# Performance work log

Measured on AMD Instinct MI355X. Metric: run time of the kernel, lower is better.

Reference implementation:

```python
import math
import jax, jax.numpy as jnp
import numpy as np

H = 1024
N2 = 32  # N // 2
L_LEN = 4096


def setup_inputs() -> dict:
    key = jax.random.key(0)
    k0, k1, k2 = jax.random.split(key, 3)
    log_dt = jax.random.uniform(k0, (H,), dtype=jnp.float32) * (
        math.log(0.1) - math.log(0.001)) + math.log(0.001)
    C_real = jax.random.normal(k1, (H, N2), dtype=jnp.float32)
    C_imag = jax.random.normal(k2, (H, N2), dtype=jnp.float32)
    log_A_real = jnp.log(0.5 * jnp.ones((H, N2), dtype=jnp.float32))
    A_imag = math.pi * jnp.tile(jnp.arange(N2, dtype=jnp.float32)[None, :], (H, 1))
    return {
        "log_dt": log_dt,
        "C_real": C_real,
        "C_imag": C_imag,
        "log_A_real": log_A_real,
        "A_imag": A_imag,
        "L": L_LEN,
    }


def reference(log_dt, C_real, C_imag, log_A_real, A_imag, L):
    dt = jnp.exp(log_dt)                                   # [H]
    A = -jnp.exp(log_A_real) + 1j * A_imag                 # [H, N2] complex
    dtA = A * dt[:, None]                                  # [H, N2]
    l = jnp.arange(L, dtype=jnp.float32)                   # [L]
    Kexp = jnp.exp(dtA[:, :, None] * l)                    # [H, N2, L] complex (Vandermonde)
    Ct = (C_real + 1j * C_imag) * (jnp.exp(dtA) - 1.0) / A  # [H, N2]
    K = 2.0 * jnp.einsum('hn,hnl->hl', Ct, Kexp).real      # [H, L]
    return K
```

## Files before the change

kernel.cpp:

```cpp
#include <hip/hip_runtime.h>


#define N2    32
#define LLEN  4096
#define BLK   512
#define TQ    256
#define CL    16
#define TOL   1e-3f

typedef float v2f __attribute__((ext_vector_type(2)));

__global__ __launch_bounds__(BLK, 8) void s4d_kernel(
    const float* __restrict__ log_dt,
    const float* __restrict__ C_real,
    const float* __restrict__ C_imag,
    const float* __restrict__ log_A_real,
    const float* __restrict__ A_imag,
    float* __restrict__ out)
{
    const int h   = blockIdx.x;
    const int tid = threadIdx.x;
    const int t   = tid & (TQ - 1);
    const int sl  = tid >> 8;

    __shared__ v2f    sT0[N2][16];
    __shared__ float4 sU1[N2][16];
    __shared__ v2f    sAB[N2];
    __shared__ v2f    sCt[N2];
    __shared__ float  sDrl2[N2];
    __shared__ double sTrev[N2];
    __shared__ float  sRed[CL][TQ];
    __shared__ float  sS, sRmax, sDrmax;
    __shared__ int    sJcut;

    if (tid < N2) {
        const int n = tid;
        const float dt = __expf(log_dt[h]);
        const float aR = -__expf(log_A_real[h * N2 + n]);
        const float aI = A_imag[h * N2 + n];
        const float dR = aR * dt;

        const double trev = (double)aI * (double)dt * 0.15915494309189535;

        double pz = trev; pz -= floor(pz);
        const float e1 = __expf(dR);
        const float zr = e1 * __builtin_amdgcn_cosf((float)pz);
        const float zi = e1 * __builtin_amdgcn_sinf((float)pz);

        const float inv = 1.0f / (aR * aR + aI * aI);
        const float nr  = zr - 1.0f;
        const float qr  = (nr * aR + zi * aI) * inv;
        const float qi  = (zi * aR - nr * aI) * inv;
        const float c_r = C_real[h * N2 + n], c_i = C_imag[h * N2 + n];
        const float Ctr = c_r * qr - c_i * qi;
        const float Cti = c_r * qi + c_i * qr;

        double p256 = trev * 256.0; p256 -= floor(p256);
        const float ew = __expf(dR * 256.0f);
        const float wx = ew * __builtin_amdgcn_cosf((float)p256);
        const float r2 = ew * ew;
        const float drl2 = dR * 1.4426950408889634f;

        sCt[n]   = (v2f){Ctr, Cti};
        sDrl2[n] = drl2;
        sTrev[n] = trev;
        sAB[n]   = (v2f){2.0f * wx, -r2};

        float S = fabsf(Ctr) + fabsf(Cti);
        float r = ew;
        float dm = drl2;
#pragma unroll
        for (int m = 16; m >= 1; m >>= 1) {
            S  += __shfl_xor(S, m, 32);
            r   = fmaxf(r,  __shfl_xor(r,  m, 32));
            dm  = fmaxf(dm, __shfl_xor(dm, m, 32));
        }
        if (n == 0) {
            sS = S; sRmax = r; sDrmax = dm;
            int jc = CL;
            if (r < 0.9999f) {
                const float tail0 = 2.0f * S / (1.0f - r);
                jc = 0;
                float rj = 1.0f;
                while (jc < CL && tail0 * rj >= TOL) { rj *= r; ++jc; }
            }
            sJcut = jc;
        }
    }
    __syncthreads();

#pragma unroll
    for (int it = 0; it < 2; ++it) {
        const int tau = tid + BLK * it;
        if (tau < 512) {
            const int n = tau >> 4, k = tau & 15;
            double p = sTrev[n] * (double)k; p -= floor(p);
            const float g = __builtin_amdgcn_exp2f(sDrl2[n] * (float)k);
            sT0[n][k] = (v2f){ g * __builtin_amdgcn_cosf((float)p),
                               g * __builtin_amdgcn_sinf((float)p) };
        } else {
            const int tu = tau - 512;
            const int n = tu >> 4, m = tu & 15;
            const v2f    Ct = sCt[n];
            const double tr = sTrev[n];
            const float  dl = sDrl2[n];

            double p0 = tr * (double)(16 * m); p0 -= floor(p0);
            const float g0 = __builtin_amdgcn_exp2f(dl * (float)(16 * m));
            const float c0 = g0 * __builtin_amdgcn_cosf((float)p0);
            const float s0 = g0 * __builtin_amdgcn_sinf((float)p0);

            double p1 = tr * (double)(16 * m + 256); p1 -= floor(p1);
            const float g1 = __builtin_amdgcn_exp2f(dl * (float)(16 * m + 256));
            const float c1 = g1 * __builtin_amdgcn_cosf((float)p1);
            const float s1 = g1 * __builtin_amdgcn_sinf((float)p1);

            sU1[n][m] = make_float4(Ct.x * c0 - Ct.y * s0,
                                    Ct.x * s0 + Ct.y * c0,
                                    Ct.x * c1 - Ct.y * s1,
                                    Ct.x * s1 + Ct.y * c1);
        }
    }
    __syncthreads();

    float acc[CL];
#pragma unroll
    for (int j = 0; j < CL; ++j) acc[j] = 0.0f;

    const int jcut = __builtin_amdgcn_readfirstlane(sJcut);
    bool active = (jcut > 0);
    {
        const float rmax = sRmax;
        if (rmax < 0.9999f) {
            const float bound = 2.0f * sS *
                __builtin_amdgcn_exp2f(sDrmax * (float)t) / (1.0f - rmax);
            if (bound < TOL) active = false;
        }
    }

    if (active) {
        const int t0 = t & 15, t1 = t >> 4;
        const int nbase = sl * 16;

        for (int ch = 0; ch < 2; ++ch) {
            const int nb = nbase + ch * 8;
            float xa[8], xb[8], ca[8], cb[8];

#pragma unroll
            for (int k = 0; k < 8; ++k) {
                const int n = nb + k;
                const v2f    b = sT0[n][t0];
                const float4 u = sU1[n][t1];
                xa[k] = __builtin_fmaf(-u.y, b.y, u.x * b.x);
                xb[k] = __builtin_fmaf(-u.w, b.y, u.z * b.x);
                const v2f ab = sAB[n];
                ca[k] = ab.x;  cb[k] = ab.y;
            }

#pragma unroll
            for (int k = 0; k < 8; ++k) acc[0] += xa[k];
            if (jcut > 1) {
#pragma unroll
                for (int k = 0; k < 8; ++k) acc[1] += xb[k];
            }

#pragma unroll
            for (int jp = 0; jp < (CL - 2) / 2; ++jp) {
                const int j = 2 + 2 * jp;
                if (j < jcut) {
#pragma unroll
                    for (int k = 0; k < 8; ++k) {
                        xa[k] = ca[k] * xb[k] + cb[k] * xa[k];
                        acc[j] += xa[k];
                    }
#pragma unroll
                    for (int k = 0; k < 8; ++k) {
                        xb[k] = ca[k] * xa[k] + cb[k] * xb[k];
                        acc[j + 1] += xb[k];
                    }
                }
            }
        }
    }

    if (sl == 0) {
#pragma unroll
        for (int j = 0; j < CL; ++j) sRed[j][t] = acc[j];
    }
    __syncthreads();
    if (sl == 1) {
#pragma unroll
        for (int j = 0; j < CL; ++j) sRed[j][t] += acc[j];
    }
    __syncthreads();

    float* __restrict__ o = out + (size_t)h * LLEN + sl * (8 * TQ) + t;
#pragma unroll
    for (int jj = 0; jj < 8; ++jj)
        o[jj * TQ] = 2.0f * sRed[8 * sl + jj][t];
}

extern "C" void kernel_launch(void* const* d_in, const int* in_sizes, int n_in,
                              void* d_out, int out_size, void* d_ws, size_t ws_size,
                              hipStream_t stream) {
    const float* log_dt     = (const float*)d_in[0];
    const float* C_real     = (const float*)d_in[1];
    const float* C_imag     = (const float*)d_in[2];
    const float* log_A_real = (const float*)d_in[3];
    const float* A_imag     = (const float*)d_in[4];
    float* out = (float*)d_out;

    const int H = in_sizes[0];
    s4d_kernel<<<dim3(H), dim3(BLK), 0, stream>>>(
        log_dt, C_real, C_imag, log_A_real, A_imag, out);
}
```

Before: 88.24 us.

## Split modes across two blocks per channel and combine with atomics

Each channel's 32 modes are now split over two 256-thread blocks (2H blocks total). Each block writes its partial sums straight to global memory with atomicAdd after the output is zeroed with a memset, replacing the shared-memory reduction and its barriers. The setup stage is also trimmed: U1 is derived from U0 by multiplying with the precomputed w = z^256 rather than doing a second exp/sincos, and the per-mode tables are packed in pairs into float4 for wider LDS reads. In exchange this adds a memset launch, global atomic traffic, and outputs beyond jcut that are left at zero from the memset.

```diff
diff --git a/kernel.cpp b/kernel.cpp
--- a/kernel.cpp
+++ b/kernel.cpp
@@ -1,11 +1,11 @@
 #include <hip/hip_runtime.h>
 
 
-#define N2    32
 #define LLEN  4096
-#define BLK   512
-#define TQ    256
+#define BLK   256
 #define CL    16
+#define NB    16
+#define NPB   8
 #define TOL   1e-3f
 
 typedef float v2f __attribute__((ext_vector_type(2)));
@@ -18,26 +18,26 @@
     const float* __restrict__ A_imag,
     float* __restrict__ out)
 {
-    const int h   = blockIdx.x;
-    const int tid = threadIdx.x;
-    const int t   = tid & (TQ - 1);
-    const int sl  = tid >> 8;
-
-    __shared__ v2f    sT0[N2][16];
-    __shared__ float4 sU1[N2][16];
-    __shared__ v2f    sAB[N2];
-    __shared__ v2f    sCt[N2];
-    __shared__ float  sDrl2[N2];
-    __shared__ double sTrev[N2];
-    __shared__ float  sRed[CL][TQ];
+    const int bx    = blockIdx.x;
+    const int h     = bx & 1023;
+    const int half  = bx >> 10;
+    const int nbase = half * NB;
+    const int t     = threadIdx.x;
+
+    __shared__ float4 sT0P[NPB][16];
+    __shared__ float4 sU1[NB][16];
+    __shared__ float4 sABP[NPB];
+    __shared__ v2f    sCt[NB], sW[NB];
+    __shared__ float  sDrl2[NB];
+    __shared__ double sTrev[NB];
     __shared__ float  sS, sRmax, sDrmax;
     __shared__ int    sJcut;
 
-    if (tid < N2) {
-        const int n = tid;
+    if (t < NB) {
+        const int n  = h * 32 + nbase + t;
         const float dt = __expf(log_dt[h]);
-        const float aR = -__expf(log_A_real[h * N2 + n]);
-        const float aI = A_imag[h * N2 + n];
+        const float aR = -__expf(log_A_real[n]);
+        const float aI = A_imag[n];
         const float dR = aR * dt;
 
         const double trev = (double)aI * (double)dt * 0.15915494309189535;
@@ -51,31 +51,35 @@
         const float nr  = zr - 1.0f;
         const float qr  = (nr * aR + zi * aI) * inv;
         const float qi  = (zi * aR - nr * aI) * inv;
-        const float c_r = C_real[h * N2 + n], c_i = C_imag[h * N2 + n];
+        const float c_r = C_real[n], c_i = C_imag[n];
         const float Ctr = c_r * qr - c_i * qi;
         const float Cti = c_r * qi + c_i * qr;
 
         double p256 = trev * 256.0; p256 -= floor(p256);
         const float ew = __expf(dR * 256.0f);
         const float wx = ew * __builtin_amdgcn_cosf((float)p256);
+        const float wy = ew * __builtin_amdgcn_sinf((float)p256);
         const float r2 = ew * ew;
         const float drl2 = dR * 1.4426950408889634f;
 
-        sCt[n]   = (v2f){Ctr, Cti};
-        sDrl2[n] = drl2;
-        sTrev[n] = trev;
-        sAB[n]   = (v2f){2.0f * wx, -r2};
-
-        float S = fabsf(Ctr) + fabsf(Cti);
-        float r = ew;
+        sCt[t]   = (v2f){Ctr, Cti};
+        sW[t]    = (v2f){wx, wy};
+        sDrl2[t] = drl2;
+        sTrev[t] = trev;
+        float* ab = (float*)&sABP[t >> 1];
+        ab[t & 1]       = 2.0f * wx;
+        ab[2 + (t & 1)] = -r2;
+
+        float S  = fabsf(Ctr) + fabsf(Cti);
+        float r  = ew;
         float dm = drl2;
 #pragma unroll
-        for (int m = 16; m >= 1; m >>= 1) {
-            S  += __shfl_xor(S, m, 32);
-            r   = fmaxf(r,  __shfl_xor(r,  m, 32));
-            dm  = fmaxf(dm, __shfl_xor(dm, m, 32));
-        }
-        if (n == 0) {
+        for (int m = 8; m >= 1; m >>= 1) {
+            S  += __shfl_xor(S, m, 16);
+            r   = fmaxf(r,  __shfl_xor(r,  m, 16));
+            dm  = fmaxf(dm, __shfl_xor(dm, m, 16));
+        }
+        if (t == 0) {
             sS = S; sRmax = r; sDrmax = dm;
             int jc = CL;
             if (r < 0.9999f) {
@@ -89,37 +93,27 @@
     }
     __syncthreads();
 
-#pragma unroll
-    for (int it = 0; it < 2; ++it) {
-        const int tau = tid + BLK * it;
-        if (tau < 512) {
-            const int n = tau >> 4, k = tau & 15;
-            double p = sTrev[n] * (double)k; p -= floor(p);
-            const float g = __builtin_amdgcn_exp2f(sDrl2[n] * (float)k);
-            sT0[n][k] = (v2f){ g * __builtin_amdgcn_cosf((float)p),
-                               g * __builtin_amdgcn_sinf((float)p) };
-        } else {
-            const int tu = tau - 512;
-            const int n = tu >> 4, m = tu & 15;
-            const v2f    Ct = sCt[n];
-            const double tr = sTrev[n];
-            const float  dl = sDrl2[n];
-
-            double p0 = tr * (double)(16 * m); p0 -= floor(p0);
-            const float g0 = __builtin_amdgcn_exp2f(dl * (float)(16 * m));
-            const float c0 = g0 * __builtin_amdgcn_cosf((float)p0);
-            const float s0 = g0 * __builtin_amdgcn_sinf((float)p0);
-
-            double p1 = tr * (double)(16 * m + 256); p1 -= floor(p1);
-            const float g1 = __builtin_amdgcn_exp2f(dl * (float)(16 * m + 256));
-            const float c1 = g1 * __builtin_amdgcn_cosf((float)p1);
-            const float s1 = g1 * __builtin_amdgcn_sinf((float)p1);
-
-            sU1[n][m] = make_float4(Ct.x * c0 - Ct.y * s0,
-                                    Ct.x * s0 + Ct.y * c0,
-                                    Ct.x * c1 - Ct.y * s1,
-                                    Ct.x * s1 + Ct.y * c1);
-        }
+    {
+        const int nl = t >> 4, k = t & 15;
+        double p = sTrev[nl] * (double)k; p -= floor(p);
+        const float g  = __builtin_amdgcn_exp2f(sDrl2[nl] * (float)k);
+        const float re = g * __builtin_amdgcn_cosf((float)p);
+        const float im = g * __builtin_amdgcn_sinf((float)p);
+        float* dst = (float*)&sT0P[nl >> 1][k] + (nl & 1) * 2;
+        dst[0] = re; dst[1] = im;
+
+        const int m = k;
+        double pu = sTrev[nl] * (double)(16 * m); pu -= floor(pu);
+        const float gu = __builtin_amdgcn_exp2f(sDrl2[nl] * (float)(16 * m));
+        const float c0 = gu * __builtin_amdgcn_cosf((float)pu);
+        const float s0 = gu * __builtin_amdgcn_sinf((float)pu);
+        const v2f Ct = sCt[nl];
+        const v2f w  = sW[nl];
+        const float u0r = Ct.x * c0 - Ct.y * s0;
+        const float u0i = Ct.x * s0 + Ct.y * c0;
+        const float u1r = u0r * w.x - u0i * w.y;
+        const float u1i = u0r * w.y + u0i * w.x;
+        sU1[nl][m] = make_float4(u0r, u0i, u1r, u1i);
     }
     __syncthreads();
 
@@ -140,21 +134,24 @@
 
     if (active) {
         const int t0 = t & 15, t1 = t >> 4;
-        const int nbase = sl * 16;
 
         for (int ch = 0; ch < 2; ++ch) {
-            const int nb = nbase + ch * 8;
             float xa[8], xb[8], ca[8], cb[8];
 
 #pragma unroll
-            for (int k = 0; k < 8; ++k) {
-                const int n = nb + k;
-                const v2f    b = sT0[n][t0];
-                const float4 u = sU1[n][t1];
-                xa[k] = __builtin_fmaf(-u.y, b.y, u.x * b.x);
-                xb[k] = __builtin_fmaf(-u.w, b.y, u.z * b.x);
-                const v2f ab = sAB[n];
-                ca[k] = ab.x;  cb[k] = ab.y;
+            for (int pp = 0; pp < 4; ++pp) {
+                const int pair = ch * 4 + pp;
+                const float4 ab = sABP[pair];
+                const float4 b  = sT0P[pair][t0];
+                const float4 u0 = sU1[2 * pair][t1];
+                const float4 u1 = sU1[2 * pair + 1][t1];
+                const int k0 = 2 * pp, k1 = k0 + 1;
+                xa[k0] = __builtin_fmaf(-u0.y, b.y, u0.x * b.x);
+                xb[k0] = __builtin_fmaf(-u0.w, b.y, u0.z * b.x);
+                xa[k1] = __builtin_fmaf(-u1.y, b.w, u1.x * b.z);
+                xb[k1] = __builtin_fmaf(-u1.w, b.w, u1.z * b.z);
+                ca[k0] = ab.x; ca[k1] = ab.y;
+                cb[k0] = ab.z; cb[k1] = ab.w;
             }
 
 #pragma unroll
@@ -181,23 +178,12 @@
                 }
             }
         }
-    }
-
-    if (sl == 0) {
-#pragma unroll
-        for (int j = 0; j < CL; ++j) sRed[j][t] = acc[j];
-    }
-    __syncthreads();
-    if (sl == 1) {
-#pragma unroll
-        for (int j = 0; j < CL; ++j) sRed[j][t] += acc[j];
-    }
-    __syncthreads();
-
-    float* __restrict__ o = out + (size_t)h * LLEN + sl * (8 * TQ) + t;
-#pragma unroll
-    for (int jj = 0; jj < 8; ++jj)
-        o[jj * TQ] = 2.0f * sRed[8 * sl + jj][t];
+
+        float* __restrict__ o = out + (size_t)h * LLEN + t;
+#pragma unroll
+        for (int j = 0; j < CL; ++j)
+            if (j < jcut) atomicAdd(&o[j * BLK], 2.0f * acc[j]);
+    }
 }
 
 extern "C" void kernel_launch(void* const* d_in, const int* in_sizes, int n_in,
@@ -211,6 +197,7 @@
     float* out = (float*)d_out;
 
     const int H = in_sizes[0];
-    s4d_kernel<<<dim3(H), dim3(BLK), 0, stream>>>(
+    hipMemsetAsync(out, 0, (size_t)out_size * sizeof(float), stream);
+    s4d_kernel<<<dim3(2 * H), dim3(BLK), 0, stream>>>(
         log_dt, C_real, C_imag, log_A_real, A_imag, out);
 }
```

New measurement: 93.11 us. 1.06x slower.
